# Performance work log

Hardware: AMD Instinct MI355X
Metric: run time of the kernel (lower is better)

## Reference

```python
import jax, jax.numpy as jnp
import numpy as np

PATCH = 16
EMBED = 384
BINS = 32
LN_EPS = 1e-5


def setup_inputs() -> dict:
    key = jax.random.key(0)
    k1, k2 = jax.random.split(key, 2)
    images = jax.random.uniform(k1, (64, 3, 224, 224), dtype=jnp.float32)  # pixels in [0,1]
    proj_w = jax.random.normal(k2, (EMBED, 3, PATCH, PATCH), dtype=jnp.float32) * 0.02  # OIHW
    proj_b = jnp.zeros((EMBED,), jnp.float32)
    ln_gamma = jnp.ones((EMBED,), jnp.float32)
    ln_beta = jnp.zeros((EMBED,), jnp.float32)
    return {"images": images, "proj_w": proj_w, "proj_b": proj_b,
            "ln_gamma": ln_gamma, "ln_beta": ln_beta}


def _patch_entropy(images, patch_size):
    # images: (B, C, H, W) in [0,1]
    B, C, H, W = images.shape
    gH, gW = H // patch_size, W // patch_size
    gray = images.mean(axis=1)  # (B, H, W)
    # non-overlapping patches -> (B, N, P*P)
    patches = gray.reshape(B, gH, patch_size, gW, patch_size)
    patches = patches.transpose(0, 1, 3, 2, 4).reshape(B, gH * gW, patch_size * patch_size)
    # quantize to 32 bins (floor, matching torch .long() on non-negative values)
    q = jnp.clip(patches * (BINS - 1), 0, BINS - 1).astype(jnp.int32)
    one_hot = jax.nn.one_hot(q, BINS, dtype=jnp.float32)      # (B, N, P*P, 32)
    hist = one_hot.sum(axis=2)                                 # (B, N, 32)
    prob = hist / jnp.maximum(hist.sum(axis=-1, keepdims=True), 1e-8)
    log_prob = jnp.log2(prob + 1e-10)
    entropy = -(prob * log_prob).sum(axis=-1)                  # (B, N)
    return entropy / np.float32(np.log2(BINS))


def reference(images, proj_w, proj_b, ln_gamma, ln_beta):
    p = PATCH
    B, C, H, W = images.shape
    gH, gW = H // p, W // p
    entropy = _patch_entropy(images, p)
    # patch-embed conv: kernel=stride=patch_size, VALID padding
    x = jax.lax.conv_general_dilated(
        images, proj_w, window_strides=(p, p), padding='VALID',
        dimension_numbers=('NCHW', 'OIHW', 'NCHW'))            # (B, D, gH, gW)
    x = x + proj_b[None, :, None, None]
    x = x.transpose(0, 2, 3, 1).reshape(B, gH * gW, -1)        # (B, N, D)
    mu = x.mean(axis=-1, keepdims=True)
    var = x.var(axis=-1, keepdims=True)                        # biased, like torch LayerNorm
    x = (x - mu) / jnp.sqrt(var + LN_EPS) * ln_gamma + ln_beta
    return x, entropy
```

## Files before the change

### kernel.cpp

```cpp
#include <hip/hip_runtime.h>

#define BATCH 64
#define GH 14
#define GW 14
#define NPATCH (GH*GW)
#define M_ROWS (BATCH*NPATCH)
#define KDIM 768
#define DDIM 384
#define HW (224*224)

typedef __attribute__((ext_vector_type(8))) short s16x8;
typedef __attribute__((ext_vector_type(4))) float f32x4;
typedef __attribute__((ext_vector_type(4))) unsigned short u16x4;

__device__ __forceinline__ unsigned short f2bf(float f) {
    unsigned int u = __float_as_uint(f);
    u += 0x7fff + ((u >> 16) & 1);
    return (unsigned short)(u >> 16);
}

__device__ __forceinline__ void load_lds16(const void* g, void* l) {
    __builtin_amdgcn_global_load_lds(
        (const __attribute__((address_space(1))) unsigned int*)g,
        (__attribute__((address_space(3))) unsigned int*)l, 16, 0, 0);
}

__global__ __launch_bounds__(256) void patch_kernel(const float* __restrict__ img,
                                                    const float* __restrict__ w,
                                                    unsigned short* __restrict__ A,
                                                    unsigned short* __restrict__ W,
                                                    float* __restrict__ ent) {
    if (blockIdx.x >= 3136) {
        int t = (blockIdx.x - 3136) * 256 + threadIdx.x;
        float4 v = ((const float4*)w)[t];
        u16x4 o = { f2bf(v.x), f2bf(v.y), f2bf(v.z), f2bf(v.w) };
        *(u16x4*)(W + t * 4) = o;
        return;
    }
    __shared__ int hist[4][32];
    const int lane = threadIdx.x & 63;
    const int wave = threadIdx.x >> 6;
    const int p = blockIdx.x * 4 + wave;
    const int b = p / NPATCH;
    const int n = p - b * NPATCH;
    const int ph = n / GW, pw = n - ph * GW;

    if (lane < 32) hist[wave][lane] = 0;
    __syncthreads();

    const int r = lane >> 2;
    const int cc = (lane & 3) * 4;
    const float* base = img + (size_t)b * (3 * HW) + (ph * 16 + r) * 224 + pw * 16 + cc;

    float4 v0 = *(const float4*)(base);
    float4 v1 = *(const float4*)(base + HW);
    float4 v2 = *(const float4*)(base + 2 * HW);

    unsigned short* arow = A + (size_t)p * KDIM;
    u16x4 o0 = { f2bf(v0.x), f2bf(v0.y), f2bf(v0.z), f2bf(v0.w) };
    u16x4 o1 = { f2bf(v1.x), f2bf(v1.y), f2bf(v1.z), f2bf(v1.w) };
    u16x4 o2 = { f2bf(v2.x), f2bf(v2.y), f2bf(v2.z), f2bf(v2.w) };
    *(u16x4*)(arow + 0 * 256 + lane * 4) = o0;
    *(u16x4*)(arow + 1 * 256 + lane * 4) = o1;
    *(u16x4*)(arow + 2 * 256 + lane * 4) = o2;

    float g[4] = { (v0.x + v1.x + v2.x) / 3.0f,
                   (v0.y + v1.y + v2.y) / 3.0f,
                   (v0.z + v1.z + v2.z) / 3.0f,
                   (v0.w + v1.w + v2.w) / 3.0f };
#pragma unroll
    for (int j = 0; j < 4; ++j) {
        int bin = (int)(g[j] * 31.0f);
        bin = bin < 0 ? 0 : (bin > 31 ? 31 : bin);
        atomicAdd(&hist[wave][bin], 1);
    }
    __syncthreads();

    float t = 0.0f;
    if (lane < 32) {
        float pr = (float)hist[wave][lane] * (1.0f / 256.0f);
        t = -pr * log2f(pr + 1e-10f);
    }
#pragma unroll
    for (int off = 32; off; off >>= 1) t += __shfl_xor(t, off);
    if (lane == 0) ent[p] = t * (1.0f / 5.0f);
}

__global__ __launch_bounds__(384) void gemm_ln_kernel(const unsigned short* __restrict__ A,
                                                      const unsigned short* __restrict__ Bt,
                                                      const float* __restrict__ bias,
                                                      const float* __restrict__ gamma,
                                                      const float* __restrict__ beta,
                                                      float* __restrict__ C) {
    __shared__ __align__(16) unsigned short SH[(64 + 384) * 64];
    __shared__ float sred[64], sred2[64], smean[64], srstd[64];
    unsigned short* As = SH;
    unsigned short* Bs = SH + 64 * 64;

    const int tid  = threadIdx.x;
    const int lane = tid & 63;
    const int w    = tid >> 6;
    const int quad = lane >> 4;
    const int cl   = lane & 15;
    const int rowBase = blockIdx.x * 64;

    if (tid < 64) { sred[tid] = 0.0f; sred2[tid] = 0.0f; }

    f32x4 acc[4][4] = {};

    for (int kt = 0; kt < KDIM; kt += 64) {
#pragma unroll
        for (int i = 0; i < 10; ++i) {
            int cb = i * 384 + w * 64;
            if (i == 9 && cb >= 3584 - 64 + 64) {  }
            if (i == 9 && w >= 2) break;
            int c = (i == 9) ? (3456 + tid) : (cb + lane);
            if (c < 512) {
                int r  = c >> 3, kss = c & 7;
                int ksg = kss ^ (r & 7);
                load_lds16(A + (size_t)(rowBase + r) * KDIM + kt + ksg * 8,
                           (unsigned short*)SH + c * 8);
            } else {
                int cc2 = c - 512;
                int n  = cc2 >> 3, kss = cc2 & 7;
                int ksg = kss ^ (n & 7);
                load_lds16(Bt + (size_t)n * KDIM + kt + ksg * 8,
                           (unsigned short*)SH + c * 8);
            }
        }
        __syncthreads();
#pragma unroll
        for (int ks = 0; ks < 2; ++ks) {
            const int sw = (ks * 4 + quad) ^ (cl & 7);
            s16x8 a_frag[4], b_frag[4];
#pragma unroll
            for (int i = 0; i < 4; ++i) {
                a_frag[i] = *(const s16x8*)(As + ((i * 16 + cl) * 8 + sw) * 8);
                b_frag[i] = *(const s16x8*)(Bs + ((w * 64 + i * 16 + cl) * 8 + sw) * 8);
            }
#pragma unroll
            for (int i = 0; i < 4; ++i)
#pragma unroll
                for (int j = 0; j < 4; ++j)
                    acc[i][j] = __builtin_amdgcn_mfma_f32_16x16x32_bf16(
                        a_frag[i], b_frag[j], acc[i][j], 0, 0, 0);
        }
        __syncthreads();
    }

    float bv[4], gv[4], btv[4];
#pragma unroll
    for (int j = 0; j < 4; ++j) {
        int col = w * 64 + j * 16 + cl;
        bv[j] = bias[col]; gv[j] = gamma[col]; btv[j] = beta[col];
    }

#pragma unroll
    for (int i = 0; i < 4; ++i) {
#pragma unroll
        for (int r = 0; r < 4; ++r) {
            float s1 = 0.0f, s2 = 0.0f;
#pragma unroll
            for (int j = 0; j < 4; ++j) {
                float v = acc[i][j][r] + bv[j];
                s1 += v; s2 += v * v;
            }
#pragma unroll
            for (int off = 1; off < 16; off <<= 1) {
                s1 += __shfl_xor(s1, off);
                s2 += __shfl_xor(s2, off);
            }
            if (cl == 0) {
                int row = i * 16 + quad * 4 + r;
                atomicAdd(&sred[row], s1);
                atomicAdd(&sred2[row], s2);
            }
        }
    }
    __syncthreads();
    if (tid < 64) {
        float mu  = sred[tid] * (1.0f / (float)DDIM);
        float var = sred2[tid] * (1.0f / (float)DDIM) - mu * mu;
        smean[tid] = mu;
        srstd[tid] = rsqrtf(var + 1e-5f);
    }
    __syncthreads();

#pragma unroll
    for (int i = 0; i < 4; ++i) {
#pragma unroll
        for (int r = 0; r < 4; ++r) {
            int row = i * 16 + quad * 4 + r;
            float mu = smean[row], rs = srstd[row];
            float* crow = C + (size_t)(rowBase + row) * DDIM;
#pragma unroll
            for (int j = 0; j < 4; ++j)
                crow[w * 64 + j * 16 + cl] = (acc[i][j][r] + bv[j] - mu) * rs * gv[j] + btv[j];
        }
    }
}

extern "C" void kernel_launch(void* const* d_in, const int* in_sizes, int n_in,
                              void* d_out, int out_size, void* d_ws, size_t ws_size,
                              hipStream_t stream) {
    const float* img = (const float*)d_in[0];
    const float* pw  = (const float*)d_in[1];
    const float* pb  = (const float*)d_in[2];
    const float* gam = (const float*)d_in[3];
    const float* bet = (const float*)d_in[4];
    float* out = (float*)d_out;

    unsigned short* Abf = (unsigned short*)d_ws;
    unsigned short* Wbf = (unsigned short*)((char*)d_ws + 19267584);
    float* ent = out + (size_t)M_ROWS * DDIM;

    hipLaunchKernelGGL(patch_kernel,   dim3(3424), dim3(256), 0, stream,
                       img, pw, Abf, Wbf, ent);
    hipLaunchKernelGGL(gemm_ln_kernel, dim3(196),  dim3(384), 0, stream,
                       Abf, Wbf, pb, gam, bet, out);
}
```

Baseline: 114.4 us.

## Fuse patch extraction and entropy into GEMM+LayerNorm kernel, drop bf16 A buffer

Patch gathering and bf16 conversion of image pixels now happen directly inside the GEMM+LayerNorm kernel when filling the A tile, so the intermediate bf16 A matrix is never written to or read back from global memory. The per-patch entropy histogram is computed in a prologue of the same kernel, and the weight cast becomes its own small kernel. This removes a large global write/read round trip. In exchange, the A tile is loaded with synchronous loads plus conversion instead of async global-to-LDS loads, the image is read twice, and the entropy work runs on only 196 blocks.

```diff
diff --git a/kernel.cpp b/kernel.cpp
--- a/kernel.cpp
+++ b/kernel.cpp
@@ -1,10 +1,7 @@
 #include <hip/hip_runtime.h>
 
-#define BATCH 64
-#define GH 14
-#define GW 14
-#define NPATCH (GH*GW)
-#define M_ROWS (BATCH*NPATCH)
+#define NPATCH 196
+#define M_ROWS 12544
 #define KDIM 768
 #define DDIM 384
 #define HW (224*224)
@@ -25,77 +22,26 @@
         (__attribute__((address_space(3))) unsigned int*)l, 16, 0, 0);
 }
 
-__global__ __launch_bounds__(256) void patch_kernel(const float* __restrict__ img,
-                                                    const float* __restrict__ w,
-                                                    unsigned short* __restrict__ A,
-                                                    unsigned short* __restrict__ W,
+__global__ __launch_bounds__(256) void wcast_kernel(const float* __restrict__ w,
+                                                    unsigned short* __restrict__ W) {
+    int t = blockIdx.x * 256 + threadIdx.x;
+    float4 v = ((const float4*)w)[t];
+    u16x4 o = { f2bf(v.x), f2bf(v.y), f2bf(v.z), f2bf(v.w) };
+    *(u16x4*)(W + t * 4) = o;
+}
+
+__global__ __launch_bounds__(384) void fused_kernel(const float* __restrict__ img,
+                                                    const unsigned short* __restrict__ Bt,
+                                                    const float* __restrict__ bias,
+                                                    const float* __restrict__ gamma,
+                                                    const float* __restrict__ beta,
+                                                    float* __restrict__ C,
                                                     float* __restrict__ ent) {
-    if (blockIdx.x >= 3136) {
-        int t = (blockIdx.x - 3136) * 256 + threadIdx.x;
-        float4 v = ((const float4*)w)[t];
-        u16x4 o = { f2bf(v.x), f2bf(v.y), f2bf(v.z), f2bf(v.w) };
-        *(u16x4*)(W + t * 4) = o;
-        return;
-    }
-    __shared__ int hist[4][32];
-    const int lane = threadIdx.x & 63;
-    const int wave = threadIdx.x >> 6;
-    const int p = blockIdx.x * 4 + wave;
-    const int b = p / NPATCH;
-    const int n = p - b * NPATCH;
-    const int ph = n / GW, pw = n - ph * GW;
-
-    if (lane < 32) hist[wave][lane] = 0;
-    __syncthreads();
-
-    const int r = lane >> 2;
-    const int cc = (lane & 3) * 4;
-    const float* base = img + (size_t)b * (3 * HW) + (ph * 16 + r) * 224 + pw * 16 + cc;
-
-    float4 v0 = *(const float4*)(base);
-    float4 v1 = *(const float4*)(base + HW);
-    float4 v2 = *(const float4*)(base + 2 * HW);
-
-    unsigned short* arow = A + (size_t)p * KDIM;
-    u16x4 o0 = { f2bf(v0.x), f2bf(v0.y), f2bf(v0.z), f2bf(v0.w) };
-    u16x4 o1 = { f2bf(v1.x), f2bf(v1.y), f2bf(v1.z), f2bf(v1.w) };
-    u16x4 o2 = { f2bf(v2.x), f2bf(v2.y), f2bf(v2.z), f2bf(v2.w) };
-    *(u16x4*)(arow + 0 * 256 + lane * 4) = o0;
-    *(u16x4*)(arow + 1 * 256 + lane * 4) = o1;
-    *(u16x4*)(arow + 2 * 256 + lane * 4) = o2;
-
-    float g[4] = { (v0.x + v1.x + v2.x) / 3.0f,
-                   (v0.y + v1.y + v2.y) / 3.0f,
-                   (v0.z + v1.z + v2.z) / 3.0f,
-                   (v0.w + v1.w + v2.w) / 3.0f };
-#pragma unroll
-    for (int j = 0; j < 4; ++j) {
-        int bin = (int)(g[j] * 31.0f);
-        bin = bin < 0 ? 0 : (bin > 31 ? 31 : bin);
-        atomicAdd(&hist[wave][bin], 1);
-    }
-    __syncthreads();
-
-    float t = 0.0f;
-    if (lane < 32) {
-        float pr = (float)hist[wave][lane] * (1.0f / 256.0f);
-        t = -pr * log2f(pr + 1e-10f);
-    }
-#pragma unroll
-    for (int off = 32; off; off >>= 1) t += __shfl_xor(t, off);
-    if (lane == 0) ent[p] = t * (1.0f / 5.0f);
-}
-
-__global__ __launch_bounds__(384) void gemm_ln_kernel(const unsigned short* __restrict__ A,
-                                                      const unsigned short* __restrict__ Bt,
-                                                      const float* __restrict__ bias,
-                                                      const float* __restrict__ gamma,
-                                                      const float* __restrict__ beta,
-                                                      float* __restrict__ C) {
-    __shared__ __align__(16) unsigned short SH[(64 + 384) * 64];
+    __shared__ __align__(16) unsigned short As[64 * 64];
+    __shared__ __align__(16) unsigned short Bs[384 * 64];
+    __shared__ int hist[6][32];
+    __shared__ int pbase[64];
     __shared__ float sred[64], sred2[64], smean[64], srstd[64];
-    unsigned short* As = SH;
-    unsigned short* Bs = SH + 64 * 64;
 
     const int tid  = threadIdx.x;
     const int lane = tid & 63;
@@ -106,27 +52,65 @@
 
     if (tid < 64) { sred[tid] = 0.0f; sred2[tid] = 0.0f; }
 
+    for (int it = 0; it < 11; ++it) {
+        int lp = w + it * 6;
+        if (lp >= 64) break;
+        if (lane < 32) hist[w][lane] = 0;
+        int p = rowBase + lp;
+        int b = p / NPATCH;
+        int n = p - b * NPATCH;
+        int ph = n / 14, pw2 = n - ph * 14;
+        int base = b * (3 * HW) + (ph * 16) * 224 + pw2 * 16;
+        if (lane == 0) pbase[lp] = base;
+        const float* q0 = img + base + (lane >> 2) * 224 + (lane & 3) * 4;
+        float4 v0 = *(const float4*)(q0);
+        float4 v1 = *(const float4*)(q0 + HW);
+        float4 v2 = *(const float4*)(q0 + 2 * HW);
+        float g[4] = { (v0.x + v1.x + v2.x) * (1.0f / 3.0f),
+                       (v0.y + v1.y + v2.y) * (1.0f / 3.0f),
+                       (v0.z + v1.z + v2.z) * (1.0f / 3.0f),
+                       (v0.w + v1.w + v2.w) * (1.0f / 3.0f) };
+#pragma unroll
+        for (int j = 0; j < 4; ++j) {
+            int bin = (int)(g[j] * 31.0f);
+            bin = bin < 0 ? 0 : (bin > 31 ? 31 : bin);
+            atomicAdd(&hist[w][bin], 1);
+        }
+        float t = 0.0f;
+        if (lane < 32) {
+            float pr = (float)hist[w][lane] * (1.0f / 256.0f);
+            t = -pr * log2f(pr + 1e-10f);
+        }
+#pragma unroll
+        for (int off = 32; off; off >>= 1) t += __shfl_xor(t, off);
+        if (lane == 0) ent[p] = t * (1.0f / 5.0f);
+    }
+    __syncthreads();
+
     f32x4 acc[4][4] = {};
 
     for (int kt = 0; kt < KDIM; kt += 64) {
 #pragma unroll
-        for (int i = 0; i < 10; ++i) {
-            int cb = i * 384 + w * 64;
-            if (i == 9 && cb >= 3584 - 64 + 64) {  }
-            if (i == 9 && w >= 2) break;
-            int c = (i == 9) ? (3456 + tid) : (cb + lane);
-            if (c < 512) {
-                int r  = c >> 3, kss = c & 7;
-                int ksg = kss ^ (r & 7);
-                load_lds16(A + (size_t)(rowBase + r) * KDIM + kt + ksg * 8,
-                           (unsigned short*)SH + c * 8);
-            } else {
-                int cc2 = c - 512;
-                int n  = cc2 >> 3, kss = cc2 & 7;
-                int ksg = kss ^ (n & 7);
-                load_lds16(Bt + (size_t)n * KDIM + kt + ksg * 8,
-                           (unsigned short*)SH + c * 8);
-            }
+        for (int i = 0; i < 8; ++i) {
+            int c = i * 384 + tid;
+            int n = c >> 3, kss = c & 7;
+            load_lds16(Bt + (size_t)n * KDIM + kt + ((kss ^ (n & 7)) * 8),
+                       (unsigned short*)Bs + c * 8);
+        }
+        const int cch = kt >> 8;
+        const int pr0 = (kt & 255) >> 4;
+#pragma unroll
+        for (int j = 0; j < 3; ++j) {
+            int f = j * 384 + tid;
+            if (j == 2 && tid >= 256) break;
+            int m = f >> 4, q = f & 15;
+            int pr = q >> 2, cg = q & 3;
+            float4 v = *(const float4*)(img + pbase[m] + cch * HW + (pr0 + pr) * 224 + cg * 4);
+            int kl = pr * 16 + cg * 4;
+            int kc = kl >> 3, half = (kl >> 2) & 1;
+            int slot = kc ^ (m & 7);
+            u16x4 o = { f2bf(v.x), f2bf(v.y), f2bf(v.z), f2bf(v.w) };
+            *(u16x4*)((char*)As + m * 128 + slot * 16 + half * 8) = o;
         }
         __syncthreads();
 #pragma unroll
@@ -135,8 +119,8 @@
             s16x8 a_frag[4], b_frag[4];
 #pragma unroll
             for (int i = 0; i < 4; ++i) {
-                a_frag[i] = *(const s16x8*)(As + ((i * 16 + cl) * 8 + sw) * 8);
-                b_frag[i] = *(const s16x8*)(Bs + ((w * 64 + i * 16 + cl) * 8 + sw) * 8);
+                a_frag[i] = *(const s16x8*)(As + (i * 16 + cl) * 64 + sw * 8);
+                b_frag[i] = *(const s16x8*)(Bs + (w * 64 + i * 16 + cl) * 64 + sw * 8);
             }
 #pragma unroll
             for (int i = 0; i < 4; ++i)
@@ -154,7 +138,6 @@
         int col = w * 64 + j * 16 + cl;
         bv[j] = bias[col]; gv[j] = gamma[col]; btv[j] = beta[col];
     }
-
 #pragma unroll
     for (int i = 0; i < 4; ++i) {
 #pragma unroll
@@ -210,12 +193,10 @@
     const float* bet = (const float*)d_in[4];
     float* out = (float*)d_out;
 
-    unsigned short* Abf = (unsigned short*)d_ws;
-    unsigned short* Wbf = (unsigned short*)((char*)d_ws + 19267584);
+    unsigned short* Wbf = (unsigned short*)d_ws;
     float* ent = out + (size_t)M_ROWS * DDIM;
 
-    hipLaunchKernelGGL(patch_kernel,   dim3(3424), dim3(256), 0, stream,
-                       img, pw, Abf, Wbf, ent);
-    hipLaunchKernelGGL(gemm_ln_kernel, dim3(196),  dim3(384), 0, stream,
-                       Abf, Wbf, pb, gam, bet, out);
-}
+    hipLaunchKernelGGL(wcast_kernel, dim3(288), dim3(256), 0, stream, pw, Wbf);
+    hipLaunchKernelGGL(fused_kernel, dim3(196), dim3(384), 0, stream,
+                       img, Wbf, pb, gam, bet, out, ent);
+}
```

Result: slower. 121.3 us (+6.0%).

## Double GEMM row tile to 128 with 768-thread blocks sharing weight tile

Applied to the files above, without the earlier changes.

The fused GEMM+LayerNorm kernel now processes 128 rows per block using 12 waves arranged 2 rows by 6 column groups, so each staged weight tile is reused across twice as many rows. This cuts redundant loads of the full weight matrix from global memory. In exchange, the grid halves to 98 blocks, leaving many compute units idle and reducing latency hiding. A minor change replaces division by 3 with multiplication by its reciprocal in the patch kernel.

```diff
diff --git a/kernel.cpp b/kernel.cpp
--- a/kernel.cpp
+++ b/kernel.cpp
@@ -1,10 +1,7 @@
 #include <hip/hip_runtime.h>
 
-#define BATCH 64
-#define GH 14
-#define GW 14
-#define NPATCH (GH*GW)
-#define M_ROWS (BATCH*NPATCH)
+#define NPATCH 196
+#define M_ROWS 12544
 #define KDIM 768
 #define DDIM 384
 #define HW (224*224)
@@ -43,7 +40,7 @@
     const int p = blockIdx.x * 4 + wave;
     const int b = p / NPATCH;
     const int n = p - b * NPATCH;
-    const int ph = n / GW, pw = n - ph * GW;
+    const int ph = n / 14, pw = n - ph * 14;
 
     if (lane < 32) hist[wave][lane] = 0;
     __syncthreads();
@@ -64,10 +61,10 @@
     *(u16x4*)(arow + 1 * 256 + lane * 4) = o1;
     *(u16x4*)(arow + 2 * 256 + lane * 4) = o2;
 
-    float g[4] = { (v0.x + v1.x + v2.x) / 3.0f,
-                   (v0.y + v1.y + v2.y) / 3.0f,
-                   (v0.z + v1.z + v2.z) / 3.0f,
-                   (v0.w + v1.w + v2.w) / 3.0f };
+    float g[4] = { (v0.x + v1.x + v2.x) * (1.0f / 3.0f),
+                   (v0.y + v1.y + v2.y) * (1.0f / 3.0f),
+                   (v0.z + v1.z + v2.z) * (1.0f / 3.0f),
+                   (v0.w + v1.w + v2.w) * (1.0f / 3.0f) };
 #pragma unroll
     for (int j = 0; j < 4; ++j) {
         int bin = (int)(g[j] * 31.0f);
@@ -86,47 +83,49 @@
     if (lane == 0) ent[p] = t * (1.0f / 5.0f);
 }
 
-__global__ __launch_bounds__(384) void gemm_ln_kernel(const unsigned short* __restrict__ A,
+__global__ __launch_bounds__(768) void gemm_ln_kernel(const unsigned short* __restrict__ A,
                                                       const unsigned short* __restrict__ Bt,
                                                       const float* __restrict__ bias,
                                                       const float* __restrict__ gamma,
                                                       const float* __restrict__ beta,
                                                       float* __restrict__ C) {
-    __shared__ __align__(16) unsigned short SH[(64 + 384) * 64];
-    __shared__ float sred[64], sred2[64], smean[64], srstd[64];
+    __shared__ __align__(16) unsigned short SH[(128 + 384) * 64];
+    __shared__ float sred[128], sred2[128], smean[128], srstd[128];
     unsigned short* As = SH;
-    unsigned short* Bs = SH + 64 * 64;
+    unsigned short* Bs = SH + 128 * 64;
 
     const int tid  = threadIdx.x;
     const int lane = tid & 63;
     const int w    = tid >> 6;
+    const int wr   = w & 1;
+    const int wc   = w >> 1;
     const int quad = lane >> 4;
     const int cl   = lane & 15;
-    const int rowBase = blockIdx.x * 64;
-
-    if (tid < 64) { sred[tid] = 0.0f; sred2[tid] = 0.0f; }
+    const int rowBase = blockIdx.x * 128;
+
+    if (tid < 128) { sred[tid] = 0.0f; sred2[tid] = 0.0f; }
 
     f32x4 acc[4][4] = {};
 
     for (int kt = 0; kt < KDIM; kt += 64) {
-#pragma unroll
-        for (int i = 0; i < 10; ++i) {
-            int cb = i * 384 + w * 64;
-            if (i == 9 && cb >= 3584 - 64 + 64) {  }
-            if (i == 9 && w >= 2) break;
-            int c = (i == 9) ? (3456 + tid) : (cb + lane);
-            if (c < 512) {
-                int r  = c >> 3, kss = c & 7;
-                int ksg = kss ^ (r & 7);
-                load_lds16(A + (size_t)(rowBase + r) * KDIM + kt + ksg * 8,
-                           (unsigned short*)SH + c * 8);
-            } else {
-                int cc2 = c - 512;
-                int n  = cc2 >> 3, kss = cc2 & 7;
-                int ksg = kss ^ (n & 7);
-                load_lds16(Bt + (size_t)n * KDIM + kt + ksg * 8,
-                           (unsigned short*)SH + c * 8);
-            }
+        {
+            int c = tid;
+            int r = c >> 3, ks = c & 7;
+            load_lds16(A + (size_t)(rowBase + r) * KDIM + kt + ((ks ^ (r & 7)) * 8),
+                       (unsigned short*)As + c * 8);
+            if (tid < 256) {
+                int c2 = 768 + tid;
+                int r2 = c2 >> 3, ks2 = c2 & 7;
+                load_lds16(A + (size_t)(rowBase + r2) * KDIM + kt + ((ks2 ^ (r2 & 7)) * 8),
+                           (unsigned short*)As + c2 * 8);
+            }
+        }
+#pragma unroll
+        for (int i = 0; i < 4; ++i) {
+            int c = i * 768 + tid;
+            int n = c >> 3, ks = c & 7;
+            load_lds16(Bt + (size_t)n * KDIM + kt + ((ks ^ (n & 7)) * 8),
+                       (unsigned short*)Bs + c * 8);
         }
         __syncthreads();
 #pragma unroll
@@ -135,8 +134,8 @@
             s16x8 a_frag[4], b_frag[4];
 #pragma unroll
             for (int i = 0; i < 4; ++i) {
-                a_frag[i] = *(const s16x8*)(As + ((i * 16 + cl) * 8 + sw) * 8);
-                b_frag[i] = *(const s16x8*)(Bs + ((w * 64 + i * 16 + cl) * 8 + sw) * 8);
+                a_frag[i] = *(const s16x8*)(As + (wr * 64 + i * 16 + cl) * 64 + sw * 8);
+                b_frag[i] = *(const s16x8*)(Bs + (wc * 64 + i * 16 + cl) * 64 + sw * 8);
             }
 #pragma unroll
             for (int i = 0; i < 4; ++i)
@@ -151,10 +150,9 @@
     float bv[4], gv[4], btv[4];
 #pragma unroll
     for (int j = 0; j < 4; ++j) {
-        int col = w * 64 + j * 16 + cl;
+        int col = wc * 64 + j * 16 + cl;
         bv[j] = bias[col]; gv[j] = gamma[col]; btv[j] = beta[col];
     }
-
 #pragma unroll
     for (int i = 0; i < 4; ++i) {
 #pragma unroll
@@ -171,14 +169,14 @@
                 s2 += __shfl_xor(s2, off);
             }
             if (cl == 0) {
-                int row = i * 16 + quad * 4 + r;
+                int row = wr * 64 + i * 16 + quad * 4 + r;
                 atomicAdd(&sred[row], s1);
                 atomicAdd(&sred2[row], s2);
             }
         }
     }
     __syncthreads();
-    if (tid < 64) {
+    if (tid < 128) {
         float mu  = sred[tid] * (1.0f / (float)DDIM);
         float var = sred2[tid] * (1.0f / (float)DDIM) - mu * mu;
         smean[tid] = mu;
@@ -190,12 +188,12 @@
     for (int i = 0; i < 4; ++i) {
 #pragma unroll
         for (int r = 0; r < 4; ++r) {
-            int row = i * 16 + quad * 4 + r;
+            int row = wr * 64 + i * 16 + quad * 4 + r;
             float mu = smean[row], rs = srstd[row];
             float* crow = C + (size_t)(rowBase + row) * DDIM;
 #pragma unroll
             for (int j = 0; j < 4; ++j)
-                crow[w * 64 + j * 16 + cl] = (acc[i][j][r] + bv[j] - mu) * rs * gv[j] + btv[j];
+                crow[wc * 64 + j * 16 + cl] = (acc[i][j][r] + bv[j] - mu) * rs * gv[j] + btv[j];
         }
     }
 }
@@ -216,6 +214,6 @@
 
     hipLaunchKernelGGL(patch_kernel,   dim3(3424), dim3(256), 0, stream,
                        img, pw, Abf, Wbf, ent);
-    hipLaunchKernelGGL(gemm_ln_kernel, dim3(196),  dim3(384), 0, stream,
+    hipLaunchKernelGGL(gemm_ln_kernel, dim3(98),   dim3(768), 0, stream,
                        Abf, Wbf, pb, gam, bet, out);
 }
```

After: 117.8 us. 2.9% more time.
